# Kernel tuning notes

Measured on AMD Instinct MI355X. Metric: run time of the kernel, lower is better.

## Reference

```python
import jax, jax.numpy as jnp
import numpy as np
import math

B, E, V, D, L = 2, 100000, 12500, 128, 4


def _ln(x, g, b, eps=1e-5):
    m = jnp.mean(x, axis=-1, keepdims=True)
    v = jnp.mean(jnp.square(x - m), axis=-1, keepdims=True)
    return (x - m) / jnp.sqrt(v + eps) * g + b


def setup_inputs() -> dict:
    key = jax.random.key(0)
    ks = jax.random.split(key, 20)
    s = 0.02
    inp = {
        "delta_noisy": jax.random.normal(ks[0], (B, E, 3), jnp.float32),
        "n": jax.random.randint(ks[1], (B,), 0, 1000, jnp.int32),
        "edge_index": jax.random.randint(ks[2], (2, E), 0, V, jnp.int32),
        "num_vertices": V,
        "w_in": jax.random.normal(ks[3], (3, D), jnp.float32) * s,
        "b_in": jnp.zeros((D,), jnp.float32),
        "W1": jax.random.normal(ks[4], (L, 2 * D, D), jnp.float32) * s,
        "b1": jnp.zeros((L, D), jnp.float32),
        "ln_g": jnp.ones((L, D), jnp.float32),
        "ln_b": jnp.zeros((L, D), jnp.float32),
        "W2": jax.random.normal(ks[5], (L, D, D), jnp.float32) * s,
        "b2": jnp.zeros((L, D), jnp.float32),
        "norm_g": jnp.ones((L, D), jnp.float32),
        "norm_b": jnp.zeros((L, D), jnp.float32),
        "te_w1": jax.random.normal(ks[6], (D, 4 * D), jnp.float32) * s,
        "te_b1": jnp.zeros((4 * D,), jnp.float32),
        "te_w2": jax.random.normal(ks[7], (4 * D, D), jnp.float32) * s,
        "te_b2": jnp.zeros((D,), jnp.float32),
        "w_out": jax.random.normal(ks[8], (D, 3), jnp.float32) * s,
        "b_out": jnp.zeros((3,), jnp.float32),
    }
    return inp


def reference(delta_noisy, n, edge_index, num_vertices, w_in, b_in, W1, b1,
              ln_g, ln_b, W2, b2, norm_g, norm_b, te_w1, te_b1, te_w2, te_b2,
              w_out, b_out):
    Bq, Eq, _ = delta_noisy.shape
    Dq = w_in.shape[1]
    src, dst = edge_index[0], edge_index[1]

    # input projection: (B,E,3) -> (B,E,D)
    h = delta_noisy @ w_in + b_in

    # sinusoidal timestep embedding + MLP
    half = Dq // 2
    freqs = jnp.exp(-math.log(10000.0) * jnp.arange(half, dtype=jnp.float32) / half)
    args = n.astype(jnp.float32)[:, None] * freqs[None, :]
    emb = jnp.concatenate([jnp.sin(args), jnp.cos(args)], axis=-1)  # (B,D)
    t_emb = jax.nn.silu(emb @ te_w1 + te_b1) @ te_w2 + te_b2
    h = h + t_emb[:, None, :]

    for i in range(W1.shape[0]):
        # scatter-add edge features into both endpoint vertices: (B,V,D)
        vf = jnp.zeros((Bq, num_vertices, Dq), h.dtype)
        vf = vf.at[:, src].add(h).at[:, dst].add(h)
        # gather back to edges and run edge MLP
        x = jnp.concatenate([vf[:, src, :], vf[:, dst, :]], axis=-1)  # (B,E,2D)
        x = x @ W1[i] + b1[i]
        x = jax.nn.silu(_ln(x, ln_g[i], ln_b[i]))
        x = x @ W2[i] + b2[i]
        h = _ln(h + x, norm_g[i], norm_b[i])

    return h @ w_out + b_out
```

## Files before the change

### kernel.cpp

```cpp
#include <hip/hip_runtime.h>
#include <math.h>

#define Bc 2
#define Ec 100000
#define Vc 12500
#define Dc 128
#define Lc 4

typedef __attribute__((ext_vector_type(4))) float f32x4;
typedef __attribute__((ext_vector_type(8))) short short8s;
typedef __attribute__((ext_vector_type(8))) __bf16 bf16x8;

static __device__ __forceinline__ short f2bf(float f) {
    unsigned u = __builtin_bit_cast(unsigned, f);
    unsigned r = (u + 0x7FFFu + ((u >> 16) & 1u)) >> 16;
    return (short)r;
}

static __device__ __forceinline__ f32x4 mfma16(short8s a, short8s b, f32x4 c) {
    return __builtin_amdgcn_mfma_f32_16x16x32_bf16(
        __builtin_bit_cast(bf16x8, a), __builtin_bit_cast(bf16x8, b), c, 0, 0, 0);
}

#define SWZ(row, bytecol) ((((row) * 256) + (bytecol)) ^ (((row) & 7) << 4))

__global__ void t_emb_kernel(const int* __restrict__ n,
                             const float* __restrict__ te_w1, const float* __restrict__ te_b1,
                             const float* __restrict__ te_w2, const float* __restrict__ te_b2,
                             float* __restrict__ t_emb) {
    const int b = blockIdx.x;
    const int t = threadIdx.x;
    __shared__ float emb[Dc];
    __shared__ float hid[4 * Dc];
    const float nf = (float)n[b];
    const int half = Dc / 2;
    {
        int j = (t < half) ? t : (t - half);
        float freq = expf(-logf(10000.0f) * (float)j / (float)half);
        float arg = nf * freq;
        emb[t] = (t < half) ? sinf(arg) : cosf(arg);
    }
    __syncthreads();
    for (int jj = 0; jj < 4; ++jj) {
        int c = t + jj * Dc;
        float acc = te_b1[c];
        for (int k = 0; k < Dc; ++k) acc += emb[k] * te_w1[k * (4 * Dc) + c];
        hid[c] = acc / (1.0f + expf(-acc));
    }
    __syncthreads();
    float acc = te_b2[t];
    for (int k = 0; k < 4 * Dc; ++k) acc += hid[k] * te_w2[k * Dc + t];
    t_emb[b * Dc + t] = acc;
}

__global__ void input_proj_kernel(const float* __restrict__ delta,
                                  const float* __restrict__ w_in, const float* __restrict__ b_in,
                                  const float* __restrict__ t_emb,
                                  float* __restrict__ h) {
    int idx = blockIdx.x * blockDim.x + threadIdx.x;
    const int total = Bc * Ec * (Dc / 4);
    if (idx >= total) return;
    int dq = idx & (Dc / 4 - 1);
    int be = idx >> 5;
    int b = be / Ec;
    const float* dd = delta + (size_t)be * 3;
    float d0 = dd[0], d1 = dd[1], d2 = dd[2];
    float4 acc = ((const float4*)b_in)[dq];
    float4 te = ((const float4*)t_emb)[b * (Dc / 4) + dq];
    float4 w0 = ((const float4*)w_in)[dq];
    float4 w1 = ((const float4*)w_in)[(Dc / 4) + dq];
    float4 w2 = ((const float4*)w_in)[2 * (Dc / 4) + dq];
    acc.x += te.x + d0 * w0.x + d1 * w1.x + d2 * w2.x;
    acc.y += te.y + d0 * w0.y + d1 * w1.y + d2 * w2.y;
    acc.z += te.z + d0 * w0.z + d1 * w1.z + d2 * w2.z;
    acc.w += te.w + d0 * w0.w + d1 * w1.w + d2 * w2.w;
    ((float4*)h)[idx] = acc;
}

__global__ void convert_w_kernel(const float* __restrict__ W1, const float* __restrict__ W2,
                                 short* __restrict__ w1f, short* __restrict__ w2f) {
    int idx = blockIdx.x * blockDim.x + threadIdx.x;
    if (idx < Lc * 32768) {
        int l = idx >> 15;
        int rm = idx & 32767;
        int j = rm & 7;
        int lane = (rm >> 3) & 63;
        int nt = (rm >> 9) & 7;
        int ks = (rm >> 12) & 7;
        int r = lane & 15, g = lane >> 4;
        int n = nt * 16 + r;
        int k = 32 * ks + 8 * g + j;
        w1f[idx] = f2bf(W1[((size_t)l * 256 + k) * 128 + n]);
    }
    if (idx < Lc * 16384) {
        int l = idx >> 14;
        int rm = idx & 16383;
        int j = rm & 7;
        int lane = (rm >> 3) & 63;
        int nt = (rm >> 9) & 7;
        int ks = (rm >> 12) & 3;
        int r = lane & 15, g = lane >> 4;
        int n = nt * 16 + r;
        int k = 32 * ks + 8 * g + j;
        w2f[idx] = f2bf(W2[((size_t)l * 128 + k) * 128 + n]);
    }
}

__global__ void csr_zero_kernel(int* __restrict__ cnt) {
    int i = blockIdx.x * blockDim.x + threadIdx.x;
    if (i < Vc) cnt[i] = 0;
}

__global__ void csr_count_kernel(const int* __restrict__ src, const int* __restrict__ dst,
                                 int* __restrict__ cnt) {
    int i = blockIdx.x * blockDim.x + threadIdx.x;
    if (i >= 2 * Ec) return;
    int v = (i < Ec) ? src[i] : dst[i - Ec];
    atomicAdd(&cnt[v], 1);
}

__global__ void csr_scan_kernel(const int* __restrict__ cnt,
                                int* __restrict__ off, int* __restrict__ cur) {
    __shared__ int part[256];
    const int t = threadIdx.x;
    const int CH = (Vc + 255) / 256;
    int s = 0;
    for (int j = 0; j < CH; ++j) {
        int i = t * CH + j;
        if (i < Vc) s += cnt[i];
    }
    part[t] = s;
    __syncthreads();
    for (int ofs = 1; ofs < 256; ofs <<= 1) {
        int y = (t >= ofs) ? part[t - ofs] : 0;
        __syncthreads();
        part[t] += y;
        __syncthreads();
    }
    int run = part[t] - s;
    for (int j = 0; j < CH; ++j) {
        int i = t * CH + j;
        if (i < Vc) {
            off[i] = run;
            cur[i] = run;
            run += cnt[i];
        }
    }
    if (t == 255) off[Vc] = run;
}

__global__ void csr_fill_kernel(const int* __restrict__ src, const int* __restrict__ dst,
                                int* __restrict__ cur, int* __restrict__ adj) {
    int i = blockIdx.x * blockDim.x + threadIdx.x;
    if (i >= 2 * Ec) return;
    int e = (i < Ec) ? i : (i - Ec);
    int v = (i < Ec) ? src[e] : dst[e];
    int p = atomicAdd(&cur[v], 1);
    adj[p] = e;
}

__global__ void gather_kernel(const float* __restrict__ h,
                              const int* __restrict__ off, const int* __restrict__ adj,
                              short* __restrict__ vf) {
    int gw = blockIdx.x * 4 + (threadIdx.x >> 6);
    if (gw >= Bc * Vc) return;
    int b = (gw >= Vc) ? 1 : 0;
    int v = gw - b * Vc;
    int lane = threadIdx.x & 63;
    int o0 = off[v], o1 = off[v + 1];
    const float2* hb = (const float2*)(h + (size_t)b * Ec * Dc);
    float2 a0 = make_float2(0.f, 0.f), a1 = a0, a2 = a0, a3 = a0;
    int j = o0;
    for (; j + 4 <= o1; j += 4) {
        int e0 = adj[j], e1 = adj[j + 1], e2 = adj[j + 2], e3 = adj[j + 3];
        float2 x0 = hb[(size_t)e0 * 64 + lane];
        float2 x1 = hb[(size_t)e1 * 64 + lane];
        float2 x2 = hb[(size_t)e2 * 64 + lane];
        float2 x3 = hb[(size_t)e3 * 64 + lane];
        a0.x += x0.x; a0.y += x0.y;
        a1.x += x1.x; a1.y += x1.y;
        a2.x += x2.x; a2.y += x2.y;
        a3.x += x3.x; a3.y += x3.y;
    }
    for (; j < o1; ++j) {
        int e = adj[j];
        float2 x = hb[(size_t)e * 64 + lane];
        a0.x += x.x; a0.y += x.y;
    }
    float sx = (a0.x + a1.x) + (a2.x + a3.x);
    float sy = (a0.y + a1.y) + (a2.y + a3.y);
    short2 w;
    w.x = f2bf(sx);
    w.y = f2bf(sy);
    ((short2*)vf)[(size_t)gw * (Dc / 2) + lane] = w;
}

__launch_bounds__(256, 2)
__global__ void edge_layer_kernel(float* __restrict__ h,
                                  const short* __restrict__ vf,
                                  const int* __restrict__ src, const int* __restrict__ dst,
                                  const short* __restrict__ w1f, const float* __restrict__ b1,
                                  const float* __restrict__ ln_g, const float* __restrict__ ln_b,
                                  const short* __restrict__ w2f, const float* __restrict__ b2,
                                  const float* __restrict__ ng, const float* __restrict__ nb,
                                  const float* __restrict__ w_out, const float* __restrict__ b_out,
                                  float* __restrict__ out) {
    __shared__ __align__(16) short x1s[256 * 128];
    char* x1b = (char*)x1s;

    const int t = threadIdx.x;
    const int w = t >> 6;
    const int lane = t & 63;
    const int r = lane & 15;
    const int g = lane >> 4;
    const int wavebase = (blockIdx.x * 4 + w) * 64;
    if (wavebase >= Bc * Ec) return;
    const int wloc = w * 64;

    const short *srow[4], *drow[4];
    #pragma unroll
    for (int mt = 0; mt < 4; ++mt) {
        int eg = wavebase + mt * 16 + r;
        int bb = (eg >= Ec) ? 1 : 0;
        int e = eg - bb * Ec;
        srow[mt] = vf + ((size_t)(bb * Vc + src[e])) * Dc;
        drow[mt] = vf + ((size_t)(bb * Vc + dst[e])) * Dc;
    }

    f32x4 acc[4][8];
    #pragma unroll
    for (int mt = 0; mt < 4; ++mt)
        #pragma unroll
        for (int nt = 0; nt < 8; ++nt) acc[mt][nt] = (f32x4){0.f, 0.f, 0.f, 0.f};

    short8s bcur[4], bnxt[4];
    #pragma unroll
    for (int mt = 0; mt < 4; ++mt) bcur[mt] = *(const short8s*)(srow[mt] + 8 * g);
    #pragma unroll
    for (int ks = 0; ks < 8; ++ks) {
        if (ks < 7) {
            int ksn = ks + 1;
            int kk = ksn & 3;
            #pragma unroll
            for (int mt = 0; mt < 4; ++mt) {
                const short* p = (ksn < 4) ? srow[mt] : drow[mt];
                bnxt[mt] = *(const short8s*)(p + 32 * kk + 8 * g);
            }
        }
        #pragma unroll
        for (int nt = 0; nt < 8; ++nt) {
            short8s afrag = *(const short8s*)(w1f + ((size_t)(ks * 8 + nt) * 64 + lane) * 8);
            acc[0][nt] = mfma16(afrag, bcur[0], acc[0][nt]);
            acc[1][nt] = mfma16(afrag, bcur[1], acc[1][nt]);
            acc[2][nt] = mfma16(afrag, bcur[2], acc[2][nt]);
            acc[3][nt] = mfma16(afrag, bcur[3], acc[3][nt]);
        }
        #pragma unroll
        for (int mt = 0; mt < 4; ++mt) bcur[mt] = bnxt[mt];
    }

    #pragma unroll
    for (int mt = 0; mt < 4; ++mt) {
        float s = 0.f, ss = 0.f;
        #pragma unroll
        for (int nt = 0; nt < 8; ++nt) {
            const float4 bb = *(const float4*)&b1[nt * 16 + 4 * g];
            acc[mt][nt][0] += bb.x; acc[mt][nt][1] += bb.y;
            acc[mt][nt][2] += bb.z; acc[mt][nt][3] += bb.w;
            #pragma unroll
            for (int i = 0; i < 4; ++i) { float v = acc[mt][nt][i]; s += v; ss += v * v; }
        }
        s += __shfl_xor(s, 16); ss += __shfl_xor(ss, 16);
        s += __shfl_xor(s, 32); ss += __shfl_xor(ss, 32);
        float mean = s * (1.0f / Dc);
        float var = ss * (1.0f / Dc) - mean * mean;
        float rstd = rsqrtf(var + 1e-5f);
        const int lrow = wloc + mt * 16 + r;
        #pragma unroll
        for (int nt = 0; nt < 8; ++nt) {
            const float4 lg = *(const float4*)&ln_g[nt * 16 + 4 * g];
            const float4 lb = *(const float4*)&ln_b[nt * 16 + 4 * g];
            float o[4];
            #pragma unroll
            for (int i = 0; i < 4; ++i) {
                float gg = (i == 0) ? lg.x : (i == 1) ? lg.y : (i == 2) ? lg.z : lg.w;
                float bb = (i == 0) ? lb.x : (i == 1) ? lb.y : (i == 2) ? lb.z : lb.w;
                float xh = (acc[mt][nt][i] - mean) * rstd * gg + bb;
                o[i] = xh / (1.0f + __expf(-xh));
            }
            short4 st;
            st.x = f2bf(o[0]); st.y = f2bf(o[1]); st.z = f2bf(o[2]); st.w = f2bf(o[3]);
            *(short4*)(x1b + SWZ(lrow, (nt * 16 + 4 * g) * 2)) = st;
        }
    }

    f32x4 acc2[4][8];
    #pragma unroll
    for (int mt = 0; mt < 4; ++mt)
        #pragma unroll
        for (int nt = 0; nt < 8; ++nt) acc2[mt][nt] = (f32x4){0.f, 0.f, 0.f, 0.f};
    #pragma unroll
    for (int ks = 0; ks < 4; ++ks) {
        short8s bf[4];
        #pragma unroll
        for (int mt = 0; mt < 4; ++mt) {
            const int lrow = wloc + mt * 16 + r;
            bf[mt] = *(const short8s*)(x1b + SWZ(lrow, (32 * ks + 8 * g) * 2));
        }
        #pragma unroll
        for (int nt = 0; nt < 8; ++nt) {
            short8s afrag = *(const short8s*)(w2f + ((size_t)(ks * 8 + nt) * 64 + lane) * 8);
            acc2[0][nt] = mfma16(afrag, bf[0], acc2[0][nt]);
            acc2[1][nt] = mfma16(afrag, bf[1], acc2[1][nt]);
            acc2[2][nt] = mfma16(afrag, bf[2], acc2[2][nt]);
            acc2[3][nt] = mfma16(afrag, bf[3], acc2[3][nt]);
        }
    }

    const bool last = (w_out != nullptr);
    #pragma unroll
    for (int mt = 0; mt < 4; ++mt) {
        const int eg = wavebase + mt * 16 + r;
        float* hrow = h + (size_t)eg * Dc;
        float s = 0.f, ss = 0.f;
        #pragma unroll
        for (int nt = 0; nt < 8; ++nt) {
            const float4 bb = *(const float4*)&b2[nt * 16 + 4 * g];
            const float4 hv = *(const float4*)(hrow + nt * 16 + 4 * g);
            acc2[mt][nt][0] += bb.x + hv.x; acc2[mt][nt][1] += bb.y + hv.y;
            acc2[mt][nt][2] += bb.z + hv.z; acc2[mt][nt][3] += bb.w + hv.w;
            #pragma unroll
            for (int i = 0; i < 4; ++i) { float v = acc2[mt][nt][i]; s += v; ss += v * v; }
        }
        s += __shfl_xor(s, 16); ss += __shfl_xor(ss, 16);
        s += __shfl_xor(s, 32); ss += __shfl_xor(ss, 32);
        float mean = s * (1.0f / Dc);
        float var = ss * (1.0f / Dc) - mean * mean;
        float rstd = rsqrtf(var + 1e-5f);
        if (!last) {
            #pragma unroll
            for (int nt = 0; nt < 8; ++nt) {
                const float4 gv = *(const float4*)&ng[nt * 16 + 4 * g];
                const float4 bv = *(const float4*)&nb[nt * 16 + 4 * g];
                float4 o;
                o.x = (acc2[mt][nt][0] - mean) * rstd * gv.x + bv.x;
                o.y = (acc2[mt][nt][1] - mean) * rstd * gv.y + bv.y;
                o.z = (acc2[mt][nt][2] - mean) * rstd * gv.z + bv.z;
                o.w = (acc2[mt][nt][3] - mean) * rstd * gv.w + bv.w;
                *(float4*)(hrow + nt * 16 + 4 * g) = o;
            }
        } else {
            float a0 = 0.f, a1 = 0.f, a2 = 0.f;
            #pragma unroll
            for (int nt = 0; nt < 8; ++nt) {
                const float4 gv = *(const float4*)&ng[nt * 16 + 4 * g];
                const float4 bv = *(const float4*)&nb[nt * 16 + 4 * g];
                #pragma unroll
                for (int i = 0; i < 4; ++i) {
                    float gg = (i == 0) ? gv.x : (i == 1) ? gv.y : (i == 2) ? gv.z : gv.w;
                    float bb = (i == 0) ? bv.x : (i == 1) ? bv.y : (i == 2) ? bv.z : bv.w;
                    float y = (acc2[mt][nt][i] - mean) * rstd * gg + bb;
                    int nidx = nt * 16 + 4 * g + i;
                    a0 += y * w_out[nidx * 3 + 0];
                    a1 += y * w_out[nidx * 3 + 1];
                    a2 += y * w_out[nidx * 3 + 2];
                }
            }
            a0 += __shfl_xor(a0, 16); a1 += __shfl_xor(a1, 16); a2 += __shfl_xor(a2, 16);
            a0 += __shfl_xor(a0, 32); a1 += __shfl_xor(a1, 32); a2 += __shfl_xor(a2, 32);
            if (g == 0) {
                out[(size_t)eg * 3 + 0] = a0 + b_out[0];
                out[(size_t)eg * 3 + 1] = a1 + b_out[1];
                out[(size_t)eg * 3 + 2] = a2 + b_out[2];
            }
        }
    }
}

extern "C" void kernel_launch(void* const* d_in, const int* in_sizes, int n_in,
                              void* d_out, int out_size, void* d_ws, size_t ws_size,
                              hipStream_t stream) {
    const float* delta = (const float*)d_in[0];
    const int* n = (const int*)d_in[1];
    const int* edge_index = (const int*)d_in[2];
    const float* w_in = (const float*)d_in[4];
    const float* b_in = (const float*)d_in[5];
    const float* W1 = (const float*)d_in[6];
    const float* b1 = (const float*)d_in[7];
    const float* ln_g = (const float*)d_in[8];
    const float* ln_b = (const float*)d_in[9];
    const float* W2 = (const float*)d_in[10];
    const float* b2 = (const float*)d_in[11];
    const float* ng = (const float*)d_in[12];
    const float* nb = (const float*)d_in[13];
    const float* te_w1 = (const float*)d_in[14];
    const float* te_b1 = (const float*)d_in[15];
    const float* te_w2 = (const float*)d_in[16];
    const float* te_b2 = (const float*)d_in[17];
    const float* w_out = (const float*)d_in[18];
    const float* b_out = (const float*)d_in[19];
    float* out = (float*)d_out;

    char* ws = (char*)d_ws;
    size_t o = 0;
    float* t_emb = (float*)(ws + o); o += 1024;
    float* h     = (float*)(ws + o); o += (size_t)Bc * Ec * Dc * 4;
    short* vf    = (short*)(ws + o); o += (size_t)Bc * Vc * Dc * 2;
    short* w1f   = (short*)(ws + o); o += (size_t)Lc * 32768 * 2;
    short* w2f   = (short*)(ws + o); o += (size_t)Lc * 16384 * 2;
    int* cnt     = (int*)(ws + o);   o += ((size_t)Vc * 4 + 255) / 256 * 256;
    int* off     = (int*)(ws + o);   o += ((size_t)(Vc + 1) * 4 + 255) / 256 * 256;
    int* cur     = (int*)(ws + o);   o += ((size_t)Vc * 4 + 255) / 256 * 256;
    int* adj     = (int*)(ws + o);   o += (size_t)2 * Ec * 4;

    const int* src = edge_index;
    const int* dst = edge_index + Ec;

    t_emb_kernel<<<Bc, Dc, 0, stream>>>(n, te_w1, te_b1, te_w2, te_b2, t_emb);
    convert_w_kernel<<<(Lc * 32768 + 255) / 256, 256, 0, stream>>>(W1, W2, w1f, w2f);

    {
        int total = Bc * Ec * (Dc / 4);
        input_proj_kernel<<<(total + 255) / 256, 256, 0, stream>>>(delta, w_in, b_in, t_emb, h);
    }

    csr_zero_kernel<<<(Vc + 255) / 256, 256, 0, stream>>>(cnt);
    csr_count_kernel<<<(2 * Ec + 255) / 256, 256, 0, stream>>>(src, dst, cnt);
    csr_scan_kernel<<<1, 256, 0, stream>>>(cnt, off, cur);
    csr_fill_kernel<<<(2 * Ec + 255) / 256, 256, 0, stream>>>(src, dst, cur, adj);

    const int eblocks = (Bc * Ec + 255) / 256;
    for (int i = 0; i < Lc; ++i) {
        gather_kernel<<<(Bc * Vc + 3) / 4, 256, 0, stream>>>(h, off, adj, vf);
        edge_layer_kernel<<<eblocks, 256, 0, stream>>>(
            h, vf, src, dst,
            w1f + (size_t)i * 32768, b1 + i * Dc,
            ln_g + i * Dc, ln_b + i * Dc,
            w2f + (size_t)i * 16384, b2 + i * Dc,
            ng + i * Dc, nb + i * Dc,
            (i == Lc - 1) ? w_out : nullptr, b_out, out);
    }
}
```

Before: 742.6 us.

## Shrink edge kernel to single-wave blocks of 32 edges with nt-major weights

Restructures the edge-layer kernel so each 64-thread block handles 32 edges (two 16-row tiles) instead of 256 edges over four waves. All gathered vertex fragments are preloaded up front, and the weight fragment layout is changed to nt-major so each output tile walks contiguous weight memory. The second GEMM is done per row tile using a small 16-row LDS buffer. The aim is more resident blocks, less LDS per block and more latency hiding for the gathers. The cost is less weight-fragment reuse across rows, so weights are reloaded more often from cache.

Measured after the change: 750.3 us. About the same (+1.0%).

```diff
diff --git a/kernel.cpp b/kernel.cpp
--- a/kernel.cpp
+++ b/kernel.cpp
@@ -82,11 +82,10 @@
     int idx = blockIdx.x * blockDim.x + threadIdx.x;
     if (idx < Lc * 32768) {
         int l = idx >> 15;
-        int rm = idx & 32767;
-        int j = rm & 7;
-        int lane = (rm >> 3) & 63;
-        int nt = (rm >> 9) & 7;
-        int ks = (rm >> 12) & 7;
+        int j = idx & 7;
+        int lane = (idx >> 3) & 63;
+        int ks = (idx >> 9) & 7;
+        int nt = (idx >> 12) & 7;
         int r = lane & 15, g = lane >> 4;
         int n = nt * 16 + r;
         int k = 32 * ks + 8 * g + j;
@@ -94,11 +93,10 @@
     }
     if (idx < Lc * 16384) {
         int l = idx >> 14;
-        int rm = idx & 16383;
-        int j = rm & 7;
-        int lane = (rm >> 3) & 63;
-        int nt = (rm >> 9) & 7;
-        int ks = (rm >> 12) & 3;
+        int j = idx & 7;
+        int lane = (idx >> 3) & 63;
+        int ks = (idx >> 9) & 3;
+        int nt = (idx >> 11) & 7;
         int r = lane & 15, g = lane >> 4;
         int n = nt * 16 + r;
         int k = 32 * ks + 8 * g + j;
@@ -195,7 +193,7 @@
     ((short2*)vf)[(size_t)gw * (Dc / 2) + lane] = w;
 }
 
-__launch_bounds__(256, 2)
+__launch_bounds__(64, 3)
 __global__ void edge_layer_kernel(float* __restrict__ h,
                                   const short* __restrict__ vf,
                                   const int* __restrict__ src, const int* __restrict__ dst,
@@ -205,21 +203,17 @@
                                   const float* __restrict__ ng, const float* __restrict__ nb,
                                   const float* __restrict__ w_out, const float* __restrict__ b_out,
                                   float* __restrict__ out) {
-    __shared__ __align__(16) short x1s[256 * 128];
+    __shared__ __align__(16) short x1s[16 * 128];
     char* x1b = (char*)x1s;
 
-    const int t = threadIdx.x;
-    const int w = t >> 6;
-    const int lane = t & 63;
+    const int lane = threadIdx.x;
     const int r = lane & 15;
     const int g = lane >> 4;
-    const int wavebase = (blockIdx.x * 4 + w) * 64;
-    if (wavebase >= Bc * Ec) return;
-    const int wloc = w * 64;
-
-    const short *srow[4], *drow[4];
+    const int wavebase = blockIdx.x * 32;
+
+    const short *srow[2], *drow[2];
     #pragma unroll
-    for (int mt = 0; mt < 4; ++mt) {
+    for (int mt = 0; mt < 2; ++mt) {
         int eg = wavebase + mt * 16 + r;
         int bb = (eg >= Ec) ? 1 : 0;
         int e = eg - bb * Ec;
@@ -227,99 +221,80 @@
         drow[mt] = vf + ((size_t)(bb * Vc + dst[e])) * Dc;
     }
 
-    f32x4 acc[4][8];
+    short8s bf[2][8];
     #pragma unroll
-    for (int mt = 0; mt < 4; ++mt)
+    for (int mt = 0; mt < 2; ++mt)
         #pragma unroll
-        for (int nt = 0; nt < 8; ++nt) acc[mt][nt] = (f32x4){0.f, 0.f, 0.f, 0.f};
-
-    short8s bcur[4], bnxt[4];
+        for (int ks = 0; ks < 4; ++ks) {
+            bf[mt][ks]     = *(const short8s*)(srow[mt] + 32 * ks + 8 * g);
+            bf[mt][4 + ks] = *(const short8s*)(drow[mt] + 32 * ks + 8 * g);
+        }
+
+    f32x4 acc[2][8];
     #pragma unroll
-    for (int mt = 0; mt < 4; ++mt) bcur[mt] = *(const short8s*)(srow[mt] + 8 * g);
+    for (int nt = 0; nt < 8; ++nt) {
+        acc[0][nt] = (f32x4){0.f, 0.f, 0.f, 0.f};
+        acc[1][nt] = (f32x4){0.f, 0.f, 0.f, 0.f};
+        #pragma unroll
+        for (int ks = 0; ks < 8; ++ks) {
+            short8s afrag = *(const short8s*)(w1f + ((size_t)(nt * 8 + ks) * 64 + lane) * 8);
+            acc[0][nt] = mfma16(afrag, bf[0][ks], acc[0][nt]);
+            acc[1][nt] = mfma16(afrag, bf[1][ks], acc[1][nt]);
+        }
+    }
+
+    const bool last = (w_out != nullptr);
+
     #pragma unroll
-    for (int ks = 0; ks < 8; ++ks) {
-        if (ks < 7) {
-            int ksn = ks + 1;
-            int kk = ksn & 3;
-            #pragma unroll
-            for (int mt = 0; mt < 4; ++mt) {
-                const short* p = (ksn < 4) ? srow[mt] : drow[mt];
-                bnxt[mt] = *(const short8s*)(p + 32 * kk + 8 * g);
-            }
-        }
+    for (int mt = 0; mt < 2; ++mt) {
+        {
+            float s = 0.f, ss = 0.f;
+            #pragma unroll
+            for (int nt = 0; nt < 8; ++nt) {
+                const float4 bb = *(const float4*)&b1[nt * 16 + 4 * g];
+                acc[mt][nt][0] += bb.x; acc[mt][nt][1] += bb.y;
+                acc[mt][nt][2] += bb.z; acc[mt][nt][3] += bb.w;
+                #pragma unroll
+                for (int i = 0; i < 4; ++i) { float v = acc[mt][nt][i]; s += v; ss += v * v; }
+            }
+            s += __shfl_xor(s, 16); ss += __shfl_xor(ss, 16);
+            s += __shfl_xor(s, 32); ss += __shfl_xor(ss, 32);
+            float mean = s * (1.0f / Dc);
+            float var = ss * (1.0f / Dc) - mean * mean;
+            float rstd = rsqrtf(var + 1e-5f);
+            #pragma unroll
+            for (int nt = 0; nt < 8; ++nt) {
+                const float4 lg = *(const float4*)&ln_g[nt * 16 + 4 * g];
+                const float4 lb = *(const float4*)&ln_b[nt * 16 + 4 * g];
+                float o[4];
+                #pragma unroll
+                for (int i = 0; i < 4; ++i) {
+                    float gg = (i == 0) ? lg.x : (i == 1) ? lg.y : (i == 2) ? lg.z : lg.w;
+                    float bb = (i == 0) ? lb.x : (i == 1) ? lb.y : (i == 2) ? lb.z : lb.w;
+                    float xh = (acc[mt][nt][i] - mean) * rstd * gg + bb;
+                    o[i] = xh / (1.0f + __expf(-xh));
+                }
+                short4 st;
+                st.x = f2bf(o[0]); st.y = f2bf(o[1]); st.z = f2bf(o[2]); st.w = f2bf(o[3]);
+                *(short4*)(x1b + SWZ(r, (nt * 16 + 4 * g) * 2)) = st;
+            }
+        }
+
+        short8s b2f[4];
+        #pragma unroll
+        for (int ks = 0; ks < 4; ++ks)
+            b2f[ks] = *(const short8s*)(x1b + SWZ(r, (32 * ks + 8 * g) * 2));
+        f32x4 acc2[8];
         #pragma unroll
         for (int nt = 0; nt < 8; ++nt) {
-            short8s afrag = *(const short8s*)(w1f + ((size_t)(ks * 8 + nt) * 64 + lane) * 8);
-            acc[0][nt] = mfma16(afrag, bcur[0], acc[0][nt]);
-            acc[1][nt] = mfma16(afrag, bcur[1], acc[1][nt]);
-            acc[2][nt] = mfma16(afrag, bcur[2], acc[2][nt]);
-            acc[3][nt] = mfma16(afrag, bcur[3], acc[3][nt]);
-        }
-        #pragma unroll
-        for (int mt = 0; mt < 4; ++mt) bcur[mt] = bnxt[mt];
-    }
-
-    #pragma unroll
-    for (int mt = 0; mt < 4; ++mt) {
-        float s = 0.f, ss = 0.f;
-        #pragma unroll
-        for (int nt = 0; nt < 8; ++nt) {
-            const float4 bb = *(const float4*)&b1[nt * 16 + 4 * g];
-            acc[mt][nt][0] += bb.x; acc[mt][nt][1] += bb.y;
-            acc[mt][nt][2] += bb.z; acc[mt][nt][3] += bb.w;
-            #pragma unroll
-            for (int i = 0; i < 4; ++i) { float v = acc[mt][nt][i]; s += v; ss += v * v; }
-        }
-        s += __shfl_xor(s, 16); ss += __shfl_xor(ss, 16);
-        s += __shfl_xor(s, 32); ss += __shfl_xor(ss, 32);
-        float mean = s * (1.0f / Dc);
-        float var = ss * (1.0f / Dc) - mean * mean;
-        float rstd = rsqrtf(var + 1e-5f);
-        const int lrow = wloc + mt * 16 + r;
-        #pragma unroll
-        for (int nt = 0; nt < 8; ++nt) {
-            const float4 lg = *(const float4*)&ln_g[nt * 16 + 4 * g];
-            const float4 lb = *(const float4*)&ln_b[nt * 16 + 4 * g];
-            float o[4];
-            #pragma unroll
-            for (int i = 0; i < 4; ++i) {
-                float gg = (i == 0) ? lg.x : (i == 1) ? lg.y : (i == 2) ? lg.z : lg.w;
-                float bb = (i == 0) ? lb.x : (i == 1) ? lb.y : (i == 2) ? lb.z : lb.w;
-                float xh = (acc[mt][nt][i] - mean) * rstd * gg + bb;
-                o[i] = xh / (1.0f + __expf(-xh));
-            }
-            short4 st;
-            st.x = f2bf(o[0]); st.y = f2bf(o[1]); st.z = f2bf(o[2]); st.w = f2bf(o[3]);
-            *(short4*)(x1b + SWZ(lrow, (nt * 16 + 4 * g) * 2)) = st;
-        }
-    }
-
-    f32x4 acc2[4][8];
-    #pragma unroll
-    for (int mt = 0; mt < 4; ++mt)
-        #pragma unroll
-        for (int nt = 0; nt < 8; ++nt) acc2[mt][nt] = (f32x4){0.f, 0.f, 0.f, 0.f};
-    #pragma unroll
-    for (int ks = 0; ks < 4; ++ks) {
-        short8s bf[4];
-        #pragma unroll
-        for (int mt = 0; mt < 4; ++mt) {
-            const int lrow = wloc + mt * 16 + r;
-            bf[mt] = *(const short8s*)(x1b + SWZ(lrow, (32 * ks + 8 * g) * 2));
-        }
-        #pragma unroll
-        for (int nt = 0; nt < 8; ++nt) {
-            short8s afrag = *(const short8s*)(w2f + ((size_t)(ks * 8 + nt) * 64 + lane) * 8);
-            acc2[0][nt] = mfma16(afrag, bf[0], acc2[0][nt]);
-            acc2[1][nt] = mfma16(afrag, bf[1], acc2[1][nt]);
-            acc2[2][nt] = mfma16(afrag, bf[2], acc2[2][nt]);
-            acc2[3][nt] = mfma16(afrag, bf[3], acc2[3][nt]);
-        }
-    }
-
-    const bool last = (w_out != nullptr);
-    #pragma unroll
-    for (int mt = 0; mt < 4; ++mt) {
+            acc2[nt] = (f32x4){0.f, 0.f, 0.f, 0.f};
+            #pragma unroll
+            for (int ks = 0; ks < 4; ++ks) {
+                short8s afrag = *(const short8s*)(w2f + ((size_t)(nt * 4 + ks) * 64 + lane) * 8);
+                acc2[nt] = mfma16(afrag, b2f[ks], acc2[nt]);
+            }
+        }
+
         const int eg = wavebase + mt * 16 + r;
         float* hrow = h + (size_t)eg * Dc;
         float s = 0.f, ss = 0.f;
@@ -327,10 +302,10 @@
         for (int nt = 0; nt < 8; ++nt) {
             const float4 bb = *(const float4*)&b2[nt * 16 + 4 * g];
             const float4 hv = *(const float4*)(hrow + nt * 16 + 4 * g);
-            acc2[mt][nt][0] += bb.x + hv.x; acc2[mt][nt][1] += bb.y + hv.y;
-            acc2[mt][nt][2] += bb.z + hv.z; acc2[mt][nt][3] += bb.w + hv.w;
-            #pragma unroll
-            for (int i = 0; i < 4; ++i) { float v = acc2[mt][nt][i]; s += v; ss += v * v; }
+            acc2[nt][0] += bb.x + hv.x; acc2[nt][1] += bb.y + hv.y;
+            acc2[nt][2] += bb.z + hv.z; acc2[nt][3] += bb.w + hv.w;
+            #pragma unroll
+            for (int i = 0; i < 4; ++i) { float v = acc2[nt][i]; s += v; ss += v * v; }
         }
         s += __shfl_xor(s, 16); ss += __shfl_xor(ss, 16);
         s += __shfl_xor(s, 32); ss += __shfl_xor(ss, 32);
@@ -343,10 +318,10 @@
                 const float4 gv = *(const float4*)&ng[nt * 16 + 4 * g];
                 const float4 bv = *(const float4*)&nb[nt * 16 + 4 * g];
                 float4 o;
-                o.x = (acc2[mt][nt][0] - mean) * rstd * gv.x + bv.x;
-                o.y = (acc2[mt][nt][1] - mean) * rstd * gv.y + bv.y;
-                o.z = (acc2[mt][nt][2] - mean) * rstd * gv.z + bv.z;
-                o.w = (acc2[mt][nt][3] - mean) * rstd * gv.w + bv.w;
+                o.x = (acc2[nt][0] - mean) * rstd * gv.x + bv.x;
+                o.y = (acc2[nt][1] - mean) * rstd * gv.y + bv.y;
+                o.z = (acc2[nt][2] - mean) * rstd * gv.z + bv.z;
+                o.w = (acc2[nt][3] - mean) * rstd * gv.w + bv.w;
                 *(float4*)(hrow + nt * 16 + 4 * g) = o;
             }
         } else {
@@ -359,7 +334,7 @@
                 for (int i = 0; i < 4; ++i) {
                     float gg = (i == 0) ? gv.x : (i == 1) ? gv.y : (i == 2) ? gv.z : gv.w;
                     float bb = (i == 0) ? bv.x : (i == 1) ? bv.y : (i == 2) ? bv.z : bv.w;
-                    float y = (acc2[mt][nt][i] - mean) * rstd * gg + bb;
+                    float y = (acc2[nt][i] - mean) * rstd * gg + bb;
                     int nidx = nt * 16 + 4 * g + i;
                     a0 += y * w_out[nidx * 3 + 0];
                     a1 += y * w_out[nidx * 3 + 1];
@@ -429,10 +404,10 @@
     csr_scan_kernel<<<1, 256, 0, stream>>>(cnt, off, cur);
     csr_fill_kernel<<<(2 * Ec + 255) / 256, 256, 0, stream>>>(src, dst, cur, adj);
 
-    const int eblocks = (Bc * Ec + 255) / 256;
+    const int eblocks = (Bc * Ec) / 32;
     for (int i = 0; i < Lc; ++i) {
         gather_kernel<<<(Bc * Vc + 3) / 4, 256, 0, stream>>>(h, off, adj, vf);
-        edge_layer_kernel<<<eblocks, 256, 0, stream>>>(
+        edge_layer_kernel<<<eblocks, 64, 0, stream>>>(
             h, vf, src, dst,
             w1f + (size_t)i * 32768, b1 + i * Dc,
             ln_g + i * Dc, ln_b + i * Dc,
```
